# Performance work log

Hardware: AMD Instinct MI355X
Metric: run time of the kernel (lower is better)

The kernel has to match this reference:

```python
import jax, jax.numpy as jnp
import numpy as np

D = 1024
H = 16
HD = D // H
FF = 4 * D
LN_EPS = 1e-5


def _layernorm(x, w, b):
    mu = jnp.mean(x, axis=-1, keepdims=True)
    var = jnp.mean(jnp.square(x - mu), axis=-1, keepdims=True)
    return (x - mu) * jax.lax.rsqrt(var + LN_EPS) * w + b


def setup_inputs() -> dict:
    key = jax.random.key(0)
    ks = jax.random.split(key, 12)
    s = 0.02
    return {
        "x": jax.random.normal(ks[0], (8, 1024, D), jnp.float32),
        "c": jax.random.normal(ks[1], (8, D), jnp.float32),
        "ln1_w": jnp.ones((D,), jnp.float32),
        "ln1_b": jnp.zeros((D,), jnp.float32),
        "ln2_w": jnp.ones((D,), jnp.float32),
        "ln2_b": jnp.zeros((D,), jnp.float32),
        "ada_w": jax.random.normal(ks[2], (D, 6 * D), jnp.float32) * s,
        "ada_b": jnp.zeros((6 * D,), jnp.float32),
        "qkv_w": jax.random.normal(ks[3], (D, 3 * D), jnp.float32) * s,
        "qkv_b": jnp.zeros((3 * D,), jnp.float32),
        "proj_w": jax.random.normal(ks[4], (D, D), jnp.float32) * s,
        "proj_b": jnp.zeros((D,), jnp.float32),
        "fc1_w": jax.random.normal(ks[5], (D, FF), jnp.float32) * s,
        "fc1_b": jnp.zeros((FF,), jnp.float32),
        "fc2_w": jax.random.normal(ks[6], (FF, D), jnp.float32) * s,
        "fc2_b": jnp.zeros((D,), jnp.float32),
    }


def reference(x, c, ln1_w, ln1_b, ln2_w, ln2_b, ada_w, ada_b,
              qkv_w, qkv_b, proj_w, proj_b, fc1_w, fc1_b, fc2_w, fc2_b):
    B, L, _ = x.shape
    # adaLN modulation: SiLU(c) @ W -> 6 chunks of (B, D)
    ssg = jax.nn.silu(c) @ ada_w + ada_b
    msa_shift, msa_scale, msa_gate, mlp_shift, mlp_scale, mlp_gate = jnp.split(ssg, 6, axis=-1)

    def modulate(h, shift, scale):
        return h * (1.0 + scale[:, None, :]) + shift[:, None, :]

    # ---- attention branch ----
    h = modulate(_layernorm(x, ln1_w, ln1_b), msa_shift, msa_scale)
    qkv = h @ qkv_w + qkv_b                      # (B, L, 3D)
    q, k, v = jnp.split(qkv, 3, axis=-1)
    q = q.reshape(B, L, H, HD).transpose(0, 2, 1, 3)   # (B, H, L, HD)
    k = k.reshape(B, L, H, HD).transpose(0, 2, 1, 3)
    v = v.reshape(B, L, H, HD).transpose(0, 2, 1, 3)
    scores = jnp.einsum("bhqd,bhkd->bhqk", q, k) / jnp.sqrt(jnp.float32(HD))
    attn = jax.nn.softmax(scores, axis=-1)
    a = jnp.einsum("bhqk,bhkd->bhqd", attn, v)   # (B, H, L, HD)
    a = a.transpose(0, 2, 1, 3).reshape(B, L, D)
    a = a @ proj_w + proj_b
    x = x + msa_gate[:, None, :] * a

    # ---- MLP branch ----
    h = modulate(_layernorm(x, ln2_w, ln2_b), mlp_shift, mlp_scale)
    h = jax.nn.gelu(h @ fc1_w + fc1_b, approximate=True)
    h = h @ fc2_w + fc2_b
    x = x + mlp_gate[:, None, :] * h
    return x
```

## Files before the change

kernel.cpp:

```cpp
#include <hip/hip_runtime.h>
#include <math.h>

#define DMODEL 1024
#define SIXD   6144
#define NHEAD  16
#define HEADD  64
#define LSEQ   1024
#define NBATCH 8
#define MROWS  8192

typedef unsigned short ushort_t;
typedef __attribute__((ext_vector_type(8))) short bf16x8;
typedef __attribute__((ext_vector_type(4))) float f32x4;

__device__ __forceinline__ unsigned short f2bf(float f) {
  unsigned int u = __float_as_uint(f);
  u += 0x7fff + ((u >> 16) & 1);
  return (unsigned short)(u >> 16);
}

__device__ __forceinline__ void gload_lds16(const void* g, void* l) {
  __builtin_amdgcn_global_load_lds(
      (const __attribute__((address_space(1))) unsigned int*)g,
      (__attribute__((address_space(3))) unsigned int*)l, 16, 0, 0);
}

__global__ void tcast_kernel(const float* __restrict__ W, ushort_t* __restrict__ WT,
                             int K, int N) {
  __shared__ float tile[32][33];
  int tx = threadIdx.x & 31, ty = threadIdx.x >> 5;
  int n0 = blockIdx.x * 32, k0 = blockIdx.y * 32;
#pragma unroll
  for (int r = 0; r < 4; ++r)
    tile[ty + 8*r][tx] = W[(size_t)(k0 + ty + 8*r) * N + n0 + tx];
  __syncthreads();
#pragma unroll
  for (int r = 0; r < 4; ++r)
    WT[(size_t)(n0 + ty + 8*r) * K + k0 + tx] = f2bf(tile[tx][ty + 8*r]);
}

__global__ __launch_bounds__(256) void vtrans_kernel(
    const ushort_t* __restrict__ qkvb, ushort_t* __restrict__ vT) {
  __shared__ ushort_t tile[128][66];
  int bh = blockIdx.x;
  int kt = blockIdx.y;
  int b = bh >> 4, h = bh & 15;
  int tid = threadIdx.x;
#pragma unroll
  for (int i = 0; i < 4; ++i) {
    int flat = tid + 256 * i;
    int r = flat >> 3, c8 = flat & 7;
    bf16x8 v = *(const bf16x8*)((const short*)qkvb +
        (size_t)(b * LSEQ + kt * 128 + r) * 3072 + 2048 + h * 64 + c8 * 8);
#pragma unroll
    for (int j = 0; j < 8; ++j) tile[r][c8 * 8 + j] = (ushort_t)v[j];
  }
  __syncthreads();
#pragma unroll
  for (int i = 0; i < 4; ++i) {
    int d = i * 16 + (tid >> 4);
    int kc = tid & 15;
    bf16x8 ov;
#pragma unroll
    for (int j = 0; j < 8; ++j) ov[j] = (short)tile[kc * 8 + j][d];
    *(bf16x8*)((short*)vT + (size_t)(bh * 64 + d) * 1024 + kt * 128 + kc * 8) = ov;
  }
}

__global__ void ada_kernel(const float* __restrict__ c, const float* __restrict__ ada_w,
                           const float* __restrict__ ada_b, float* __restrict__ ssg) {
  __shared__ float s[DMODEL];
  int b = blockIdx.y;
  int j = blockIdx.x * 256 + threadIdx.x;
  for (int i = threadIdx.x; i < DMODEL; i += 256) {
    float v = c[b * DMODEL + i];
    s[i] = v / (1.0f + __expf(-v));
  }
  __syncthreads();
  float acc = ada_b[j];
#pragma unroll 8
  for (int k = 0; k < DMODEL; ++k)
    acc = fmaf(s[k], ada_w[(size_t)k * SIXD + j], acc);
  ssg[b * SIXD + j] = acc;
}

__global__ __launch_bounds__(256) void ln_mod_kernel(
    const float* __restrict__ xin, const float* __restrict__ lw,
    const float* __restrict__ lb, const float* __restrict__ ssg,
    int shift_off, int scale_off, ushort_t* __restrict__ outB) {
  int row = blockIdx.x;
  int b = row >> 10;
  int tid = threadIdx.x;
  float4 v = ((const float4*)xin)[(size_t)row * 256 + tid];
  float sum = v.x + v.y + v.z + v.w;
  float sq  = v.x*v.x + v.y*v.y + v.z*v.z + v.w*v.w;
#pragma unroll
  for (int m = 32; m; m >>= 1) { sum += __shfl_xor(sum, m); sq += __shfl_xor(sq, m); }
  __shared__ float rbuf[8];
  int w = tid >> 6, lane = tid & 63;
  if (lane == 0) { rbuf[w] = sum; rbuf[4 + w] = sq; }
  __syncthreads();
  sum = rbuf[0] + rbuf[1] + rbuf[2] + rbuf[3];
  sq  = rbuf[4] + rbuf[5] + rbuf[6] + rbuf[7];
  float mu  = sum * (1.0f / 1024.0f);
  float var = sq * (1.0f / 1024.0f) - mu * mu;
  float rs  = rsqrtf(var + 1e-5f);
  const float* sg = ssg + b * SIXD;
  float vv[4] = {v.x, v.y, v.z, v.w};
  ushort4 pk;
  unsigned short* pks = (unsigned short*)&pk;
#pragma unroll
  for (int j = 0; j < 4; ++j) {
    int d = tid * 4 + j;
    float h = (vv[j] - mu) * rs * lw[d] + lb[d];
    h = h * (1.0f + sg[scale_off + d]) + sg[shift_off + d];
    pks[j] = f2bf(h);
  }
  ((ushort4*)outB)[(size_t)row * 256 + tid] = pk;
}

template <int EPI>
__global__ __launch_bounds__(256, 2) void gemm_kernel(
    const ushort_t* __restrict__ A, const ushort_t* __restrict__ BT,
    const float* __restrict__ bias, const float* __restrict__ ssg,
    const float* resid, float* outF, ushort_t* __restrict__ outB,
    int N, int K, int gate_off, int gxs) {
  __shared__ __align__(16) char SM[65536];
  int tid = threadIdx.x, lane = tid & 63, w = tid >> 6;
  int l15 = lane & 15, g = lane >> 4;
  int orig = blockIdx.x;
  int xcd = orig & 7;
  int idx = orig >> 3;
  int bxi = idx & ((1 << gxs) - 1);
  int byl = (idx >> gxs) & 7;
  int bxg = idx >> (gxs + 3);
  int bx = (bxg << gxs) + bxi;
  int by = (xcd << 3) + byl;
  int m0 = by * 128, n0 = bx * 128;
  int wrow = (w >> 1) * 64, wcol = (w & 1) * 64;
  f32x4 zero = {0.f, 0.f, 0.f, 0.f};
  f32x4 acc[4][4];
#pragma unroll
  for (int i = 0; i < 4; ++i)
#pragma unroll
    for (int j = 0; j < 4; ++j) acc[i][j] = zero;

  const char* asrc[4];
  const char* bsrc[4];
#pragma unroll
  for (int ch = 0; ch < 4; ++ch) {
    int flat = ch * 4096 + tid * 16;
    int row = flat >> 7;
    int colb = (flat & 127) ^ ((row & 7) << 4);
    asrc[ch] = (const char*)A  + ((size_t)(m0 + row) * K) * 2 + colb;
    bsrc[ch] = (const char*)BT + ((size_t)(n0 + row) * K) * 2 + colb;
  }

  int T = K >> 6;
#pragma unroll
  for (int ch = 0; ch < 4; ++ch)
    gload_lds16(asrc[ch], SM + ch * 4096 + tid * 16);
#pragma unroll
  for (int ch = 0; ch < 4; ++ch)
    gload_lds16(bsrc[ch], SM + 16384 + ch * 4096 + tid * 16);

  for (int t = 0; t < T; ++t) {
    if (t + 1 < T) {
      char* base = SM + ((t + 1) & 1) * 32768;
      size_t ko = (size_t)(t + 1) * 128;
#pragma unroll
      for (int ch = 0; ch < 4; ++ch)
        gload_lds16(asrc[ch] + ko, base + ch * 4096 + tid * 16);
#pragma unroll
      for (int ch = 0; ch < 4; ++ch)
        gload_lds16(bsrc[ch] + ko, base + 16384 + ch * 4096 + tid * 16);
      asm volatile("s_waitcnt vmcnt(8)" ::: "memory");
    } else {
      asm volatile("s_waitcnt vmcnt(0)" ::: "memory");
    }
    asm volatile("s_barrier" ::: "memory");
    const char* ab = SM + (t & 1) * 32768;
    const char* bb = ab + 16384;
#pragma unroll
    for (int kk = 0; kk < 2; ++kk) {
      bf16x8 af[4], bfr[4];
#pragma unroll
      for (int i = 0; i < 4; ++i) {
        int ar = wrow + i * 16 + l15;
        af[i]  = *(const bf16x8*)(ab + ar * 128 + ((kk * 64 + g * 16) ^ ((ar & 7) << 4)));
        int br = wcol + i * 16 + l15;
        bfr[i] = *(const bf16x8*)(bb + br * 128 + ((kk * 64 + g * 16) ^ ((br & 7) << 4)));
      }
#pragma unroll
      for (int i = 0; i < 4; ++i)
#pragma unroll
        for (int j = 0; j < 4; ++j)
          acc[i][j] = __builtin_amdgcn_mfma_f32_16x16x32_bf16(af[i], bfr[j], acc[i][j], 0, 0, 0);
    }
    asm volatile("s_barrier" ::: "memory");
  }
#pragma unroll
  for (int i = 0; i < 4; ++i)
#pragma unroll
    for (int j = 0; j < 4; ++j)
#pragma unroll
      for (int r = 0; r < 4; ++r) {
        int grow = m0 + wrow + i * 16 + g * 4 + r;
        int gcol = n0 + wcol + j * 16 + l15;
        float v = acc[i][j][r] + bias[gcol];
        if (EPI == 0) {
          outB[(size_t)grow * N + gcol] = f2bf(v);
        } else if (EPI == 1 || EPI == 3) {
          int bb2 = grow >> 10;
          float gate = ssg[bb2 * SIXD + gate_off + gcol];
          size_t idx2 = (size_t)grow * N + gcol;
          outF[idx2] = resid[idx2] + gate * v;
        } else {
          float u = v;
          float t2 = 0.7978845608028654f * (u + 0.044715f * u * u * u);
          float e = __expf(2.0f * t2);
          float th = 1.0f - 2.0f / (e + 1.0f);
          outB[(size_t)grow * N + gcol] = f2bf(0.5f * u * (1.0f + th));
        }
      }
}

__global__ __launch_bounds__(256, 2) void attn_kernel(
    const ushort_t* __restrict__ qkv,
    const ushort_t* __restrict__ vT,
    ushort_t* __restrict__ aout) {
  __shared__ __align__(16) char SM[49408];
  float* lbuf = (float*)(SM + 49152);
  int tid = threadIdx.x, lane = tid & 63, w = tid >> 6;
  int l15 = lane & 15, g = lane >> 4;
  int qt = blockIdx.x, bh = blockIdx.y;
  int b = bh >> 4, h = bh & 15;
  const float sc = 0.18033688f;

  bf16x8 aq[2], aq2[2];
  {
    int qrow = qt * 128 + w * 16 + l15;
    const short* qp = (const short*)qkv + (size_t)(b * LSEQ + qrow) * 3072 + h * 64 + g * 8;
    aq[0] = *(const bf16x8*)qp;
    aq[1] = *(const bf16x8*)(qp + 32);
    const short* qp2 = qp + (size_t)64 * 3072;
    aq2[0] = *(const bf16x8*)qp2;
    aq2[1] = *(const bf16x8*)(qp2 + 32);
#pragma unroll
    for (int ks = 0; ks < 2; ++ks) {
#pragma unroll
      for (int s = 0; s < 2; ++s) {
        union { bf16x8 v; unsigned short u[8]; } qi, qo;
        qi.v = s ? aq2[ks] : aq[ks];
#pragma unroll
        for (int j = 0; j < 8; j += 2) {
          float lo = __uint_as_float((unsigned)qi.u[j] << 16) * sc;
          float hi = __uint_as_float((unsigned)qi.u[j + 1] << 16) * sc;
          unsigned pkd;
          asm("v_cvt_pk_bf16_f32 %0, %1, %2" : "=v"(pkd) : "v"(lo), "v"(hi));
          qo.u[j] = (unsigned short)(pkd & 0xffff);
          qo.u[j + 1] = (unsigned short)(pkd >> 16);
        }
        if (s) aq2[ks] = qo.v; else aq[ks] = qo.v;
      }
    }
  }

  const char* ksrc[2];
  const char* vsrc[2];
#pragma unroll
  for (int p = 0; p < 2; ++p) {
    int flat = p * 4096 + w * 1024 + lane * 16;
    int row = flat >> 7;
    int colb = (flat & 127) ^ ((row & 7) << 4);
    ksrc[p] = (const char*)qkv + ((size_t)(b * LSEQ + row) * 3072 + 1024 + h * 64) * 2 + colb;
    vsrc[p] = (const char*)vT + ((size_t)(bh * 64 + row) * 1024) * 2 + colb;
  }

  auto STAGE = [&](int tt, int s) {
    size_t koff = (size_t)tt * (64 * 3072 * 2);
    size_t voff = (size_t)tt * 128;
#pragma unroll
    for (int p = 0; p < 2; ++p) {
      gload_lds16(ksrc[p] + koff, SM + s * 8192 + p * 4096 + w * 1024);
      gload_lds16(vsrc[p] + voff, SM + 24576 + s * 8192 + p * 4096 + w * 1024);
    }
  };

  f32x4 zero = {0.f, 0.f, 0.f, 0.f};
  f32x4 o[4] = {zero, zero, zero, zero};
  f32x4 o2[4] = {zero, zero, zero, zero};
  float lrow = 0.f, lrow2 = 0.f;

  STAGE(0, 0);
  STAGE(1, 1);
  asm volatile("s_waitcnt vmcnt(4)" ::: "memory");
  asm volatile("s_barrier" ::: "memory");

  int s0 = 0;
  for (int t = 0; t < 16; ++t) {
    int s2 = s0 + 2; if (s2 >= 3) s2 -= 3;
    if (t + 2 < 16) STAGE(t + 2, s2);
    f32x4 s4[4] = {zero, zero, zero, zero};
    f32x4 s4b[4] = {zero, zero, zero, zero};
    __builtin_amdgcn_s_setprio(1);
#pragma unroll
    for (int c = 0; c < 4; ++c)
#pragma unroll
      for (int ks = 0; ks < 2; ++ks) {
        int key = c * 16 + l15;
        bf16x8 ak = *(const bf16x8*)(SM + s0 * 8192 + key * 128 +
                                     ((ks * 64 + g * 16) ^ ((key & 7) << 4)));
        s4[c]  = __builtin_amdgcn_mfma_f32_16x16x32_bf16(ak, aq[ks],  s4[c],  0, 0, 0);
        s4b[c] = __builtin_amdgcn_mfma_f32_16x16x32_bf16(ak, aq2[ks], s4b[c], 0, 0, 0);
      }
    __builtin_amdgcn_s_setprio(0);
    unsigned pa[2][4], pa2[2][4];
    int gl = (g & 1) * 2;
#pragma unroll
    for (int s = 0; s < 2; ++s) {
      float p16[16], sump = 0.f;
#pragma unroll
      for (int c = 0; c < 4; ++c)
#pragma unroll
        for (int r = 0; r < 4; ++r) {
          float p = exp2f(s ? s4b[c][r] : s4[c][r]);
          p16[c * 4 + r] = p;
          sump += p;
        }
      if (s) lrow2 += sump; else lrow += sump;
      unsigned pk[8];
#pragma unroll
      for (int c = 0; c < 4; ++c)
#pragma unroll
        for (int m = 0; m < 2; ++m)
          asm("v_cvt_pk_bf16_f32 %0, %1, %2"
              : "=v"(pk[c * 2 + m]) : "v"(p16[c * 4 + 2 * m]), "v"(p16[c * 4 + 2 * m + 1]));
#pragma unroll
      for (int kb = 0; kb < 2; ++kb)
#pragma unroll
        for (int wv = 0; wv < 4; ++wv) {
          int srcl = l15 + (gl + (wv >> 1)) * 16;
          unsigned vA = (unsigned)__shfl((int)pk[kb * 4 + (wv & 1)], srcl);
          unsigned vB = (unsigned)__shfl((int)pk[kb * 4 + 2 + (wv & 1)], srcl);
          if (s) pa2[kb][wv] = (g >> 1) ? vB : vA;
          else   pa[kb][wv]  = (g >> 1) ? vB : vA;
        }
    }
    union PU { unsigned u[4]; bf16x8 v; };
    PU pu[2], pu2[2];
#pragma unroll
    for (int kb = 0; kb < 2; ++kb)
#pragma unroll
      for (int i = 0; i < 4; ++i) { pu[kb].u[i] = pa[kb][i]; pu2[kb].u[i] = pa2[kb][i]; }
    __builtin_amdgcn_s_setprio(1);
#pragma unroll
    for (int kb = 0; kb < 2; ++kb)
#pragma unroll
      for (int nb = 0; nb < 4; ++nb) {
        int d = nb * 16 + l15;
        bf16x8 bv = *(const bf16x8*)(SM + 24576 + s0 * 8192 + d * 128 +
                                     ((kb * 64 + g * 16) ^ ((d & 7) << 4)));
        o[nb]  = __builtin_amdgcn_mfma_f32_16x16x32_bf16(pu[kb].v,  bv, o[nb],  0, 0, 0);
        o2[nb] = __builtin_amdgcn_mfma_f32_16x16x32_bf16(pu2[kb].v, bv, o2[nb], 0, 0, 0);
      }
    __builtin_amdgcn_s_setprio(0);
    if (t + 2 < 16)      asm volatile("s_waitcnt vmcnt(4)" ::: "memory");
    else if (t + 1 < 16) asm volatile("s_waitcnt vmcnt(0)" ::: "memory");
    if (t + 1 < 16)      asm volatile("s_barrier" ::: "memory");
    s0 = s0 + 1; if (s0 >= 3) s0 -= 3;
  }
  lrow  += __shfl_xor(lrow, 16);  lrow  += __shfl_xor(lrow, 32);
  lrow2 += __shfl_xor(lrow2, 16); lrow2 += __shfl_xor(lrow2, 32);
#pragma unroll
  for (int s = 0; s < 2; ++s) {
    float inv = 1.0f / (s ? lrow2 : lrow);
    if (lane < 16) lbuf[w * 16 + lane] = inv;
    f32x4 rl = *(const f32x4*)&lbuf[w * 16 + g * 4];
#pragma unroll
    for (int nb = 0; nb < 4; ++nb)
#pragma unroll
      for (int r = 0; r < 4; ++r) {
        int qrow = qt * 128 + s * 64 + w * 16 + g * 4 + r;
        const f32x4& oo = s ? o2[nb] : o[nb];
        aout[(size_t)(b * LSEQ + qrow) * 1024 + h * 64 + nb * 16 + l15] =
            f2bf(oo[r] * rl[r]);
      }
  }
}

extern "C" void kernel_launch(void* const* d_in, const int* in_sizes, int n_in,
                              void* d_out, int out_size, void* d_ws, size_t ws_size,
                              hipStream_t stream) {
  const float* x      = (const float*)d_in[0];
  const float* c      = (const float*)d_in[1];
  const float* ln1_w  = (const float*)d_in[2];
  const float* ln1_b  = (const float*)d_in[3];
  const float* ln2_w  = (const float*)d_in[4];
  const float* ln2_b  = (const float*)d_in[5];
  const float* ada_w  = (const float*)d_in[6];
  const float* ada_b  = (const float*)d_in[7];
  const float* qkv_w  = (const float*)d_in[8];
  const float* qkv_b  = (const float*)d_in[9];
  const float* proj_w = (const float*)d_in[10];
  const float* proj_b = (const float*)d_in[11];
  const float* fc1_w  = (const float*)d_in[12];
  const float* fc1_b  = (const float*)d_in[13];
  const float* fc2_w  = (const float*)d_in[14];
  const float* fc2_b  = (const float*)d_in[15];
  float* out = (float*)d_out;
  char* ws = (char*)d_ws;

  ushort_t* qkvT  = (ushort_t*)(ws + 0);
  ushort_t* projT = (ushort_t*)(ws + 6291456);
  ushort_t* fc1T  = (ushort_t*)(ws + 8388608);
  ushort_t* fc2T  = (ushort_t*)(ws + 16777216);
  float*    ssg   = (float*)(ws + 25165824);
  ushort_t* hbuf  = (ushort_t*)(ws + 25362432);
  ushort_t* abuf  = hbuf;
  ushort_t* qkvb  = (ushort_t*)(ws + 42139648);
  ushort_t* vTb   = (ushort_t*)(ws + 92471296);
  if (ws_size < (size_t)109248512) return;

  tcast_kernel<<<dim3(96, 32),  256, 0, stream>>>(qkv_w,  qkvT, 1024, 3072);
  tcast_kernel<<<dim3(32, 32),  256, 0, stream>>>(proj_w, projT, 1024, 1024);
  tcast_kernel<<<dim3(128, 32), 256, 0, stream>>>(fc1_w,  fc1T, 1024, 4096);
  tcast_kernel<<<dim3(32, 128), 256, 0, stream>>>(fc2_w,  fc2T, 4096, 1024);
  ada_kernel<<<dim3(24, 8), 256, 0, stream>>>(c, ada_w, ada_b, ssg);

  ln_mod_kernel<<<8192, 256, 0, stream>>>(x, ln1_w, ln1_b, ssg, 0, 1024, hbuf);
  gemm_kernel<0><<<1536, 256, 0, stream>>>(hbuf, qkvT, qkv_b, nullptr,
                                           nullptr, nullptr, qkvb, 3072, 1024, 0, 2);
  vtrans_kernel<<<dim3(128, 8), 256, 0, stream>>>(qkvb, vTb);
  attn_kernel<<<dim3(8, 128), 256, 0, stream>>>(qkvb, vTb, abuf);
  gemm_kernel<1><<<512, 256, 0, stream>>>(abuf, projT, proj_b, ssg,
                                          x, out, nullptr, 1024, 1024, 2048, 2);
  ln_mod_kernel<<<8192, 256, 0, stream>>>(out, ln2_w, ln2_b, ssg, 3072, 4096, hbuf);
  gemm_kernel<2><<<2048, 256, 0, stream>>>(hbuf, fc1T, fc1_b, nullptr,
                                           nullptr, nullptr, qkvb, 4096, 1024, 0, 2);
  gemm_kernel<3><<<512, 256, 0, stream>>>(qkvb, fc2T, fc2_b, ssg,
                                          out, out, nullptr, 1024, 4096, 5120, 1);
}
```

Baseline: 415.7 us.

## Use three-stage K=32 LDS pipeline in GEMM with higher occupancy

Reworks the GEMM main loop from a double-buffered K=64 tile into a triple-buffered K=32 tile. Prefetch now runs two stages ahead with a single barrier per iteration. LDS drops from 64KB to 48KB so launch bounds can request three blocks per CU, and MFMA issue is wrapped in s_setprio to favour compute waves. The trade-off is twice as many loop iterations with fewer MFMAs each, more frequent barriers and waitcnts, and register pressure under the tighter occupancy bound.

```diff
diff --git a/kernel.cpp b/kernel.cpp
--- a/kernel.cpp
+++ b/kernel.cpp
@@ -120,12 +120,12 @@
 }
 
 template <int EPI>
-__global__ __launch_bounds__(256, 2) void gemm_kernel(
+__global__ __launch_bounds__(256, 3) void gemm_kernel(
     const ushort_t* __restrict__ A, const ushort_t* __restrict__ BT,
     const float* __restrict__ bias, const float* __restrict__ ssg,
     const float* resid, float* outF, ushort_t* __restrict__ outB,
     int N, int K, int gate_off, int gxs) {
-  __shared__ __align__(16) char SM[65536];
+  __shared__ __align__(16) char SM[49152];
   int tid = threadIdx.x, lane = tid & 63, w = tid >> 6;
   int l15 = lane & 15, g = lane >> 4;
   int orig = blockIdx.x;
@@ -145,59 +145,58 @@
 #pragma unroll
     for (int j = 0; j < 4; ++j) acc[i][j] = zero;
 
-  const char* asrc[4];
-  const char* bsrc[4];
-#pragma unroll
-  for (int ch = 0; ch < 4; ++ch) {
+  const char* asrc[2];
+  const char* bsrc[2];
+#pragma unroll
+  for (int ch = 0; ch < 2; ++ch) {
     int flat = ch * 4096 + tid * 16;
-    int row = flat >> 7;
-    int colb = (flat & 127) ^ ((row & 7) << 4);
+    int row = flat >> 6;
+    int colb = (flat & 63) ^ ((row & 3) << 4);
     asrc[ch] = (const char*)A  + ((size_t)(m0 + row) * K) * 2 + colb;
     bsrc[ch] = (const char*)BT + ((size_t)(n0 + row) * K) * 2 + colb;
   }
 
-  int T = K >> 6;
-#pragma unroll
-  for (int ch = 0; ch < 4; ++ch)
-    gload_lds16(asrc[ch], SM + ch * 4096 + tid * 16);
-#pragma unroll
-  for (int ch = 0; ch < 4; ++ch)
-    gload_lds16(bsrc[ch], SM + 16384 + ch * 4096 + tid * 16);
-
+  auto STAGE = [&](int tt, int s) {
+    size_t ko = (size_t)tt * 64;
+    char* base = SM + s * 16384;
+#pragma unroll
+    for (int ch = 0; ch < 2; ++ch) {
+      gload_lds16(asrc[ch] + ko, base + ch * 4096 + tid * 16);
+      gload_lds16(bsrc[ch] + ko, base + 8192 + ch * 4096 + tid * 16);
+    }
+  };
+
+  int T = K >> 5;
+  STAGE(0, 0);
+  STAGE(1, 1);
+  asm volatile("s_waitcnt vmcnt(4)" ::: "memory");
+  asm volatile("s_barrier" ::: "memory");
+
+  int s0 = 0;
   for (int t = 0; t < T; ++t) {
-    if (t + 1 < T) {
-      char* base = SM + ((t + 1) & 1) * 32768;
-      size_t ko = (size_t)(t + 1) * 128;
-#pragma unroll
-      for (int ch = 0; ch < 4; ++ch)
-        gload_lds16(asrc[ch] + ko, base + ch * 4096 + tid * 16);
-#pragma unroll
-      for (int ch = 0; ch < 4; ++ch)
-        gload_lds16(bsrc[ch] + ko, base + 16384 + ch * 4096 + tid * 16);
-      asm volatile("s_waitcnt vmcnt(8)" ::: "memory");
-    } else {
-      asm volatile("s_waitcnt vmcnt(0)" ::: "memory");
+    int s2 = s0 + 2; if (s2 >= 3) s2 -= 3;
+    if (t + 2 < T) STAGE(t + 2, s2);
+    const char* ab = SM + s0 * 16384;
+    const char* bb = ab + 8192;
+    bf16x8 af[4], bfr[4];
+#pragma unroll
+    for (int i = 0; i < 4; ++i) {
+      int ar = wrow + i * 16 + l15;
+      af[i]  = *(const bf16x8*)(ab + ar * 64 + ((g * 16) ^ ((ar & 3) << 4)));
+      int br = wcol + i * 16 + l15;
+      bfr[i] = *(const bf16x8*)(bb + br * 64 + ((g * 16) ^ ((br & 3) << 4)));
     }
-    asm volatile("s_barrier" ::: "memory");
-    const char* ab = SM + (t & 1) * 32768;
-    const char* bb = ab + 16384;
-#pragma unroll
-    for (int kk = 0; kk < 2; ++kk) {
-      bf16x8 af[4], bfr[4];
-#pragma unroll
-      for (int i = 0; i < 4; ++i) {
-        int ar = wrow + i * 16 + l15;
-        af[i]  = *(const bf16x8*)(ab + ar * 128 + ((kk * 64 + g * 16) ^ ((ar & 7) << 4)));
-        int br = wcol + i * 16 + l15;
-        bfr[i] = *(const bf16x8*)(bb + br * 128 + ((kk * 64 + g * 16) ^ ((br & 7) << 4)));
-      }
-#pragma unroll
-      for (int i = 0; i < 4; ++i)
-#pragma unroll
-        for (int j = 0; j < 4; ++j)
-          acc[i][j] = __builtin_amdgcn_mfma_f32_16x16x32_bf16(af[i], bfr[j], acc[i][j], 0, 0, 0);
-    }
-    asm volatile("s_barrier" ::: "memory");
+    __builtin_amdgcn_s_setprio(1);
+#pragma unroll
+    for (int i = 0; i < 4; ++i)
+#pragma unroll
+      for (int j = 0; j < 4; ++j)
+        acc[i][j] = __builtin_amdgcn_mfma_f32_16x16x32_bf16(af[i], bfr[j], acc[i][j], 0, 0, 0);
+    __builtin_amdgcn_s_setprio(0);
+    if (t + 2 < T)      asm volatile("s_waitcnt vmcnt(4)" ::: "memory");
+    else if (t + 1 < T) asm volatile("s_waitcnt vmcnt(0)" ::: "memory");
+    if (t + 1 < T)      asm volatile("s_barrier" ::: "memory");
+    s0 = s0 + 1; if (s0 >= 3) s0 -= 3;
   }
 #pragma unroll
   for (int i = 0; i < 4; ++i)
```

New measurement: 454.4 us. 9.3% more time.
